# Performance work log

Hardware: AMD Instinct MI355X
Metric: run time of the kernel (lower is better)

## Reference

```python
import jax, jax.numpy as jnp
import numpy as np

B, D, O = 256, 256, 1024

def setup_inputs() -> dict:
    key = jax.random.key(0)
    k1, k2 = jax.random.split(key)
    inputs = jax.random.normal(k1, (B, D, D), dtype=jnp.float32)
    # glorot_uniform for kernel (D, O)
    limit = float(np.sqrt(6.0 / (D + O)))
    kernel = jax.random.uniform(k2, (D, O), dtype=jnp.float32, minval=-limit, maxval=limit)
    return {"inputs": inputs, "kernel": kernel}

def reference(inputs, kernel):
    # out[b,o] = sum_i kernel[i,o] * (inputs[b] @ kernel)[i,o]  == diag(K^T Cov_b K)
    tmp = jnp.matmul(inputs, kernel)          # (B, D, O)
    return jnp.sum(kernel * tmp, axis=1)      # (B, O)
```

## Files before the change

kernel.cpp:

```cpp
#include <hip/hip_runtime.h>
#include <hip/hip_bf16.h>

typedef __attribute__((ext_vector_type(8))) short bf16x8;
typedef __attribute__((ext_vector_type(4))) float f32x4;

__device__ __forceinline__ ushort f2bf(float x) {
  unsigned u = __float_as_uint(x);
  u = (u + 0x7FFFu + ((u >> 16) & 1u)) >> 16;
  return (ushort)u;
}

__global__ void WV_kconv(const float* __restrict__ K, ushort* __restrict__ KtP) {
  int c = blockIdx.x * 256 + threadIdx.x;
  int otile = c >> 9, ks = (c >> 6) & 7, lane = c & 63;
  int o = otile * 16 + (lane & 15);
  int kb = ks * 32 + (lane >> 4) * 8;
  bf16x8 w;
  #pragma unroll
  for (int e = 0; e < 8; ++e)
    w[e] = (short)f2bf(K[(size_t)(kb + e) * 1024 + o]);
  *reinterpret_cast<bf16x8*>(KtP + (size_t)c * 8) = w;
}

__global__ __launch_bounds__(512, 2) void WV_main(
    const float* __restrict__ A, const ushort* __restrict__ KtP,
    float* __restrict__ out) {
  __shared__ short As[64 * 256];
  const int bh = blockIdx.x;
  const int b = bh >> 2, h = bh & 3;
  const float* Ah = A + (size_t)b * 65536 + (size_t)h * 16384;
  const int t = threadIdx.x;

  #pragma unroll 1
  for (int it = 0; it < 4; ++it) {
    int c = it * 512 + t;
    int m = c >> 5;
    int s = c & 31;
    const float4* p = reinterpret_cast<const float4*>(Ah) + c * 2;
    float4 v0 = p[0], v1 = p[1];
    bf16x8 w;
    w[0] = (short)f2bf(v0.x); w[1] = (short)f2bf(v0.y);
    w[2] = (short)f2bf(v0.z); w[3] = (short)f2bf(v0.w);
    w[4] = (short)f2bf(v1.x); w[5] = (short)f2bf(v1.y);
    w[6] = (short)f2bf(v1.z); w[7] = (short)f2bf(v1.w);
    int byteoff = m * 512 + ((s * 16) ^ ((m & 7) << 6));
    *reinterpret_cast<bf16x8*>(reinterpret_cast<char*>(As) + byteoff) = w;
  }
  __syncthreads();

  const int wave = t >> 6, lane = t & 63;
  const int lo = lane & 15;
  const int hi = lane >> 4;
  const ushort* KtL = KtP + lane * 8;

  #pragma unroll 1
  for (int og = 0; og < 2; ++og) {
    float oseg[4] = {0.f, 0.f, 0.f, 0.f};
    const int otb = wave * 8 + og * 4;

    f32x4 acc[4][4];
    #pragma unroll
    for (int a1 = 0; a1 < 4; ++a1)
      #pragma unroll
      for (int a2 = 0; a2 < 4; ++a2)
        acc[a1][a2] = (f32x4){0.f, 0.f, 0.f, 0.f};

    bf16x8 B0[4], B1[4];
    #pragma unroll
    for (int ot = 0; ot < 4; ++ot)
      B0[ot] = *reinterpret_cast<const bf16x8*>(
          KtL + __builtin_amdgcn_readfirstlane((otb + ot) * 4096));

    #pragma unroll 1
    for (int kp = 0; kp < 4; ++kp) {
      const int ks0 = kp * 2, ks1 = kp * 2 + 1;
      #pragma unroll
      for (int ot = 0; ot < 4; ++ot)
        B1[ot] = *reinterpret_cast<const bf16x8*>(
            KtL + __builtin_amdgcn_readfirstlane((otb + ot) * 4096 + ks1 * 512));
      __builtin_amdgcn_s_setprio(1);
      #pragma unroll
      for (int itl = 0; itl < 4; ++itl) {
        int m = itl * 16 + lo;
        int byteoff = m * 512 + ((ks0 * 64 + hi * 16) ^ ((m & 7) << 6));
        bf16x8 Af = *reinterpret_cast<const bf16x8*>(
            reinterpret_cast<char*>(As) + byteoff);
        #pragma unroll
        for (int ot = 0; ot < 4; ++ot)
          acc[itl][ot] = __builtin_amdgcn_mfma_f32_16x16x32_bf16(
              Af, B0[ot], acc[itl][ot], 0, 0, 0);
      }
      __builtin_amdgcn_s_setprio(0);
      if (kp < 3) {
        #pragma unroll
        for (int ot = 0; ot < 4; ++ot)
          B0[ot] = *reinterpret_cast<const bf16x8*>(
              KtL + __builtin_amdgcn_readfirstlane((otb + ot) * 4096 +
                                                   (ks0 + 2) * 512));
      }
      __builtin_amdgcn_s_setprio(1);
      #pragma unroll
      for (int itl = 0; itl < 4; ++itl) {
        int m = itl * 16 + lo;
        int byteoff = m * 512 + ((ks1 * 64 + hi * 16) ^ ((m & 7) << 6));
        bf16x8 Af = *reinterpret_cast<const bf16x8*>(
            reinterpret_cast<char*>(As) + byteoff);
        #pragma unroll
        for (int ot = 0; ot < 4; ++ot)
          acc[itl][ot] = __builtin_amdgcn_mfma_f32_16x16x32_bf16(
              Af, B1[ot], acc[itl][ot], 0, 0, 0);
      }
      __builtin_amdgcn_s_setprio(0);
    }

    #pragma unroll
    for (int itl = 0; itl < 4; ++itl) {
      const int kse = h * 2 + (itl >> 1);
      const int g = (itl & 1) * 2 + (hi >> 1);
      const int e = (hi & 1) * 4;
      #pragma unroll
      for (int ot = 0; ot < 4; ++ot) {
        const ushort* wp = KtP +
            ((size_t)((otb + ot) * 8 + kse) * 64 + lo + g * 16) * 8 + e;
        ushort4 wv = *reinterpret_cast<const ushort4*>(wp);
        f32x4 a = acc[itl][ot];
        float s = __uint_as_float((unsigned)wv.x << 16) * a[0]
                + __uint_as_float((unsigned)wv.y << 16) * a[1]
                + __uint_as_float((unsigned)wv.z << 16) * a[2]
                + __uint_as_float((unsigned)wv.w << 16) * a[3];
        s += __shfl_xor(s, 16);
        s += __shfl_xor(s, 32);
        oseg[ot] += s;
      }
    }

    if (lane < 16) {
      #pragma unroll
      for (int ot = 0; ot < 4; ++ot)
        atomicAdd(&out[(size_t)b * 1024 + (otb + ot) * 16 + lane], oseg[ot]);
    }
  }
}

extern "C" void kernel_launch(void* const* d_in, const int* in_sizes, int n_in,
                              void* d_out, int out_size, void* d_ws, size_t ws_size,
                              hipStream_t stream) {
  const float* A = (const float*)d_in[0];
  const float* K = (const float*)d_in[1];
  float* out = (float*)d_out;
  ushort* KtP = (ushort*)d_ws;
  hipMemsetAsync(d_out, 0, (size_t)out_size * sizeof(float), stream);
  WV_kconv<<<128, 256, 0, stream>>>(K, KtP);
  WV_main<<<1024, 512, 0, stream>>>(A, KtP, out);
}
```

Baseline: 54.56 us.

## Switch main GEMM to 32x32x16 bf16 MFMA with matching K layout

Replaces the 16x16x32 MFMA tiles with 32x32x16 MFMA instructions, so each wave now computes 2x2 tiles of 32x32 over 16 k-steps. The packed kernel layout, the LDS swizzle and the epilogue reduction are reworked to match the 32-wide fragment layout. The aim is fewer MFMA issues, fewer B-fragment loads and fewer shuffles and atomics per output. In exchange the k-loop has twice as many iterations and each instruction has a longer dependency latency.

Result: slower. 61.32 us (+12.4%).

```diff
diff --git a/kernel.cpp b/kernel.cpp
--- a/kernel.cpp
+++ b/kernel.cpp
@@ -2,7 +2,7 @@
 #include <hip/hip_bf16.h>
 
 typedef __attribute__((ext_vector_type(8))) short bf16x8;
-typedef __attribute__((ext_vector_type(4))) float f32x4;
+typedef __attribute__((ext_vector_type(16))) float f32x16;
 
 __device__ __forceinline__ ushort f2bf(float x) {
   unsigned u = __float_as_uint(x);
@@ -10,20 +10,20 @@
   return (ushort)u;
 }
 
-__global__ void WV_kconv(const float* __restrict__ K, ushort* __restrict__ KtP) {
+__global__ void WV_kconv(const float* __restrict__ K, ushort* __restrict__ KtQ) {
   int c = blockIdx.x * 256 + threadIdx.x;
-  int otile = c >> 9, ks = (c >> 6) & 7, lane = c & 63;
-  int o = otile * 16 + (lane & 15);
-  int kb = ks * 32 + (lane >> 4) * 8;
+  int otile = c >> 10, ks16 = (c >> 6) & 15, lane = c & 63;
+  int o = otile * 32 + (lane & 31);
+  int kb = ks16 * 16 + (lane >> 5) * 8;
   bf16x8 w;
   #pragma unroll
   for (int e = 0; e < 8; ++e)
     w[e] = (short)f2bf(K[(size_t)(kb + e) * 1024 + o]);
-  *reinterpret_cast<bf16x8*>(KtP + (size_t)c * 8) = w;
+  *reinterpret_cast<bf16x8*>(KtQ + (size_t)c * 8) = w;
 }
 
 __global__ __launch_bounds__(512, 2) void WV_main(
-    const float* __restrict__ A, const ushort* __restrict__ KtP,
+    const float* __restrict__ A, const ushort* __restrict__ KtQ,
     float* __restrict__ out) {
   __shared__ short As[64 * 256];
   const int bh = blockIdx.x;
@@ -43,101 +43,96 @@
     w[2] = (short)f2bf(v0.z); w[3] = (short)f2bf(v0.w);
     w[4] = (short)f2bf(v1.x); w[5] = (short)f2bf(v1.y);
     w[6] = (short)f2bf(v1.z); w[7] = (short)f2bf(v1.w);
-    int byteoff = m * 512 + ((s * 16) ^ ((m & 7) << 6));
+    int byteoff = m * 512 + ((s * 16) ^ ((m & 15) << 5));
     *reinterpret_cast<bf16x8*>(reinterpret_cast<char*>(As) + byteoff) = w;
   }
   __syncthreads();
 
   const int wave = t >> 6, lane = t & 63;
-  const int lo = lane & 15;
-  const int hi = lane >> 4;
-  const ushort* KtL = KtP + lane * 8;
+  const int lo32 = lane & 31;
+  const int hi1 = lane >> 5;
+  const ushort* KtL = KtQ + lane * 8;
 
   #pragma unroll 1
   for (int og = 0; og < 2; ++og) {
-    float oseg[4] = {0.f, 0.f, 0.f, 0.f};
-    const int otb = wave * 8 + og * 4;
+    const int otb = wave * 4 + og * 2;
 
-    f32x4 acc[4][4];
+    f32x16 acc[2][2];
     #pragma unroll
-    for (int a1 = 0; a1 < 4; ++a1)
+    for (int a1 = 0; a1 < 2; ++a1)
       #pragma unroll
-      for (int a2 = 0; a2 < 4; ++a2)
-        acc[a1][a2] = (f32x4){0.f, 0.f, 0.f, 0.f};
+      for (int a2 = 0; a2 < 2; ++a2)
+        acc[a1][a2] = (f32x16)(0.f);
 
-    bf16x8 B0[4], B1[4];
+    bf16x8 B0[2], B1[2];
     #pragma unroll
-    for (int ot = 0; ot < 4; ++ot)
+    for (int ot = 0; ot < 2; ++ot)
       B0[ot] = *reinterpret_cast<const bf16x8*>(
-          KtL + __builtin_amdgcn_readfirstlane((otb + ot) * 4096));
+          KtL + __builtin_amdgcn_readfirstlane(((otb + ot) * 16 + 0) * 512));
 
     #pragma unroll 1
-    for (int kp = 0; kp < 4; ++kp) {
+    for (int kp = 0; kp < 8; ++kp) {
       const int ks0 = kp * 2, ks1 = kp * 2 + 1;
       #pragma unroll
-      for (int ot = 0; ot < 4; ++ot)
+      for (int ot = 0; ot < 2; ++ot)
         B1[ot] = *reinterpret_cast<const bf16x8*>(
-            KtL + __builtin_amdgcn_readfirstlane((otb + ot) * 4096 + ks1 * 512));
+            KtL + __builtin_amdgcn_readfirstlane(((otb + ot) * 16 + ks1) * 512));
       __builtin_amdgcn_s_setprio(1);
       #pragma unroll
-      for (int itl = 0; itl < 4; ++itl) {
-        int m = itl * 16 + lo;
-        int byteoff = m * 512 + ((ks0 * 64 + hi * 16) ^ ((m & 7) << 6));
+      for (int itl = 0; itl < 2; ++itl) {
+        int m = itl * 32 + lo32;
+        int byteoff = m * 512 + ((ks0 * 32 + hi1 * 16) ^ ((m & 15) << 5));
         bf16x8 Af = *reinterpret_cast<const bf16x8*>(
             reinterpret_cast<char*>(As) + byteoff);
         #pragma unroll
-        for (int ot = 0; ot < 4; ++ot)
-          acc[itl][ot] = __builtin_amdgcn_mfma_f32_16x16x32_bf16(
+        for (int ot = 0; ot < 2; ++ot)
+          acc[itl][ot] = __builtin_amdgcn_mfma_f32_32x32x16_bf16(
               Af, B0[ot], acc[itl][ot], 0, 0, 0);
       }
       __builtin_amdgcn_s_setprio(0);
-      if (kp < 3) {
+      if (kp < 7) {
         #pragma unroll
-        for (int ot = 0; ot < 4; ++ot)
+        for (int ot = 0; ot < 2; ++ot)
           B0[ot] = *reinterpret_cast<const bf16x8*>(
-              KtL + __builtin_amdgcn_readfirstlane((otb + ot) * 4096 +
-                                                   (ks0 + 2) * 512));
+              KtL + __builtin_amdgcn_readfirstlane(((otb + ot) * 16 + ks0 + 2) * 512));
       }
       __builtin_amdgcn_s_setprio(1);
       #pragma unroll
-      for (int itl = 0; itl < 4; ++itl) {
-        int m = itl * 16 + lo;
-        int byteoff = m * 512 + ((ks1 * 64 + hi * 16) ^ ((m & 7) << 6));
+      for (int itl = 0; itl < 2; ++itl) {
+        int m = itl * 32 + lo32;
+        int byteoff = m * 512 + ((ks1 * 32 + hi1 * 16) ^ ((m & 15) << 5));
         bf16x8 Af = *reinterpret_cast<const bf16x8*>(
             reinterpret_cast<char*>(As) + byteoff);
         #pragma unroll
-        for (int ot = 0; ot < 4; ++ot)
-          acc[itl][ot] = __builtin_amdgcn_mfma_f32_16x16x32_bf16(
+        for (int ot = 0; ot < 2; ++ot)
+          acc[itl][ot] = __builtin_amdgcn_mfma_f32_32x32x16_bf16(
               Af, B1[ot], acc[itl][ot], 0, 0, 0);
       }
       __builtin_amdgcn_s_setprio(0);
     }
 
     #pragma unroll
-    for (int itl = 0; itl < 4; ++itl) {
-      const int kse = h * 2 + (itl >> 1);
-      const int g = (itl & 1) * 2 + (hi >> 1);
-      const int e = (hi & 1) * 4;
+    for (int ot = 0; ot < 2; ++ot) {
+      float s = 0.f;
       #pragma unroll
-      for (int ot = 0; ot < 4; ++ot) {
-        const ushort* wp = KtP +
-            ((size_t)((otb + ot) * 8 + kse) * 64 + lo + g * 16) * 8 + e;
-        ushort4 wv = *reinterpret_cast<const ushort4*>(wp);
-        f32x4 a = acc[itl][ot];
-        float s = __uint_as_float((unsigned)wv.x << 16) * a[0]
-                + __uint_as_float((unsigned)wv.y << 16) * a[1]
-                + __uint_as_float((unsigned)wv.z << 16) * a[2]
-                + __uint_as_float((unsigned)wv.w << 16) * a[3];
-        s += __shfl_xor(s, 16);
-        s += __shfl_xor(s, 32);
-        oseg[ot] += s;
+      for (int itl = 0; itl < 2; ++itl) {
+        #pragma unroll
+        for (int rq = 0; rq < 4; ++rq) {
+          const int kse = h * 4 + itl * 2 + (rq >> 1);
+          const ushort* wp = KtQ +
+              ((size_t)((otb + ot) * 16 + kse) * 64 + ((rq & 1) << 5) + lo32) * 8
+              + 4 * hi1;
+          ushort4 wv = *reinterpret_cast<const ushort4*>(wp);
+          const int rb = rq * 4;
+          s += __uint_as_float((unsigned)wv.x << 16) * acc[itl][ot][rb + 0]
+             + __uint_as_float((unsigned)wv.y << 16) * acc[itl][ot][rb + 1]
+             + __uint_as_float((unsigned)wv.z << 16) * acc[itl][ot][rb + 2]
+             + __uint_as_float((unsigned)wv.w << 16) * acc[itl][ot][rb + 3];
+        }
       }
-    }
-
-    if (lane < 16) {
-      #pragma unroll
-      for (int ot = 0; ot < 4; ++ot)
-        atomicAdd(&out[(size_t)b * 1024 + (otb + ot) * 16 + lane], oseg[ot]);
+      s += __shfl_xor(s, 32);
+      if (lane < 32)
+        atomicAdd(&out[(size_t)b * 1024 + (otb + ot) * 32 + lane], s);
     }
   }
 }
@@ -148,8 +143,8 @@
   const float* A = (const float*)d_in[0];
   const float* K = (const float*)d_in[1];
   float* out = (float*)d_out;
-  ushort* KtP = (ushort*)d_ws;
+  ushort* KtQ = (ushort*)d_ws;
   hipMemsetAsync(d_out, 0, (size_t)out_size * sizeof(float), stream);
-  WV_kconv<<<128, 256, 0, stream>>>(K, KtP);
-  WV_main<<<1024, 512, 0, stream>>>(A, KtP, out);
+  WV_kconv<<<128, 256, 0, stream>>>(K, KtQ);
+  WV_main<<<1024, 512, 0, stream>>>(A, KtQ, out);
 }
```
